# Performance work log

Measured on AMD Instinct MI355X. Metric: run time of the kernel, lower is better.

## Reference

```python
import jax, jax.numpy as jnp
import numpy as np

BOHR_RADIUS = 0.529177  # Angstrom
KE_KCAL = 332.0636      # Coulomb constant, kcal/mol * Angstrom / e^2
EPS = 1e-15
R_CUT = 5.0

ZBL = {'d': [0.8854 * BOHR_RADIUS], 'z_exp': [0.23],
       'c': [0.1818, 0.5099, 0.2802, 0.02817],
       'exponents': [3.2, 0.9423, 0.4028, 0.2016]}

def _inv_softplus(v):
    v = np.asarray(v, dtype=np.float32)
    return jnp.asarray(np.log(np.exp(v) - 1.0).reshape(-1, 1))

def setup_inputs() -> dict:
    key = jax.random.key(0)
    k1, k2, k3, k4 = jax.random.split(key, 4)
    N, E, M = 200000, 8000000, 1000
    xyz = jax.random.normal(k1, (N, 3), dtype=jnp.float32) * 3.0
    z = jax.random.randint(k2, (N,), 1, 94, dtype=jnp.int32)
    nbrs = jax.random.randint(k3, (E, 2), 0, N, dtype=jnp.int32)
    offsets = jax.random.normal(k4, (E, 3), dtype=jnp.float32) * 2.0
    num_atoms = jnp.full((M,), N // M, dtype=jnp.int32)
    return {
        'xyz': xyz, 'z': z, 'nbrs': nbrs, 'num_atoms': num_atoms, 'offsets': offsets,
        'd_inv': _inv_softplus(ZBL['d']),
        'z_exp_inv': _inv_softplus(ZBL['z_exp']),
        'c_inv': _inv_softplus(ZBL['c']),
        'exponents_inv': _inv_softplus(ZBL['exponents']),
    }

def reference(xyz, z, nbrs, num_atoms, offsets, d_inv, z_exp_inv, c_inv, exponents_inv):
    sp = jax.nn.softplus
    d, z_exp, c, exponents = sp(d_inv), sp(z_exp_inv), sp(c_inv), sp(exponents_inv)

    i, j = nbrs[:, 0], nbrs[:, 1]
    mask = j > i  # undirected-edge filter (masked instead of gathered: same math)

    z_i = z[i].astype(jnp.float32)  # [E]
    z_j = z[j].astype(jnp.float32)
    diff = xyz[i] - xyz[j] - offsets                  # [E,3]
    r_ij = jnp.sqrt((diff ** 2 + EPS).sum(-1))        # stable norm, [E]

    # ZBL phi: d,z_exp are [1,1]; broadcast over edges
    a = (d / (z_i ** z_exp + z_j ** z_exp)).reshape(-1)           # [E]
    phi = (c * jnp.exp(-exponents * r_ij / a)).sum(0) / c.sum()   # [4,E] -> [E]

    # SpookyNet cutoff, NaN-safe outside r_cut
    den = (R_CUT - r_ij) * (R_CUT + r_ij)
    safe_den = jnp.where(r_ij < R_CUT, den, 1.0)
    f_cut = jnp.where(r_ij < R_CUT, jnp.exp(-r_ij ** 2 / safe_den), 0.0)

    pairwise = KE_KCAL * z_i * z_j / r_ij * phi * f_cut
    pairwise = jnp.where(mask, pairwise, 0.0)

    N = xyz.shape[0]
    M = num_atoms.shape[0]
    mol_idx = jnp.repeat(jnp.arange(M), num_atoms, total_repeat_length=N)  # [N]
    seg = mol_idx[i]                                                       # [E]
    energy = jax.ops.segment_sum(pairwise, seg, num_segments=M).reshape(-1, 1)
    return energy
```

## Files before the change

kernel.cpp:

```cpp
#include <hip/hip_runtime.h>
#include <hip/hip_bf16.h>

#define KE_F     332.0636f
#define MAX_M    1024
#define BLK      256
#define NBLK_MAX 2048

__device__ __forceinline__ float softplusf(float x) {
    return logf(1.0f + expf(x));
}

__global__ void scan_params_kernel(const int* __restrict__ num_atoms, int M,
                                   const float* __restrict__ d_inv,
                                   const float* __restrict__ z_exp_inv,
                                   const float* __restrict__ c_inv,
                                   const float* __restrict__ exp_inv,
                                   int* __restrict__ mol_starts,
                                   float* __restrict__ params) {
    __shared__ int buf[MAX_M];
    int t = threadIdx.x;
    buf[t] = (t < M) ? num_atoms[t] : 0;
    __syncthreads();
    for (int off = 1; off < MAX_M; off <<= 1) {
        int x = (t >= off) ? buf[t - off] : 0;
        __syncthreads();
        buf[t] += x;
        __syncthreads();
    }
    if (t == 0) mol_starts[0] = 0;
    if (t < M) mol_starts[t + 1] = buf[t];
    if (t == 0) {
        float dd = softplusf(d_inv[0]);
        float c0 = softplusf(c_inv[0]), c1 = softplusf(c_inv[1]);
        float c2 = softplusf(c_inv[2]), c3 = softplusf(c_inv[3]);
        float e0 = softplusf(exp_inv[0]), e1 = softplusf(exp_inv[1]);
        float e2 = softplusf(exp_inv[2]), e3 = softplusf(exp_inv[3]);
        float ic = 1.0f / (c0 + c1 + c2 + c3);
        float id = 1.0f / dd;
        params[0] = c0 * ic; params[1] = c1 * ic; params[2] = c2 * ic; params[3] = c3 * ic;
        params[4] = e0 * id; params[5] = e1 * id; params[6] = e2 * id; params[7] = e3 * id;
        params[8] = softplusf(z_exp_inv[0]);
    }
}

__global__ void pack_kernel(const float* __restrict__ xyz,
                            const int* __restrict__ z,
                            const int* __restrict__ mol_starts, int M, int N,
                            const float* __restrict__ params,
                            float4* __restrict__ pack,
                            float2* __restrict__ aux) {
    int a = blockIdx.x * blockDim.x + threadIdx.x;
    if (a >= N) return;
    float zf = (float)z[a];
    pack[a] = make_float4(xyz[3 * a + 0], xyz[3 * a + 1], xyz[3 * a + 2], zf);
    int lo = 0, hi = M;
    while (hi - lo > 1) {
        int mid = (lo + hi) >> 1;
        if (mol_starts[mid] <= a) lo = mid; else hi = mid;
    }
    aux[a] = make_float2(__powf(zf, params[8]), __int_as_float(lo));
}

__global__ __launch_bounds__(256) void nr_main_kernel(
    const long long* __restrict__ nbrs,
    const float* __restrict__ offsets,
    const float4* __restrict__ pack,
    const float2* __restrict__ aux,
    const float* __restrict__ params,
    float* __restrict__ part, int E) {
    __shared__ float sm[MAX_M];
    for (int t = threadIdx.x; t < MAX_M; t += BLK) sm[t] = 0.0f;
    __syncthreads();

    const float4 kk = *(const float4*)(params + 0);
    const float4 gg = *(const float4*)(params + 4);

    const int stride = gridDim.x * BLK;
    for (int e = blockIdx.x * BLK + threadIdx.x; e < E; e += stride) {
        const long long nb = __builtin_nontemporal_load(nbrs + e);
        const int i = (int)nb;
        const int j = (int)(nb >> 32);
        if (j <= i) continue;

        const float ox = __builtin_nontemporal_load(offsets + 3 * e + 0);
        const float oy = __builtin_nontemporal_load(offsets + 3 * e + 1);
        const float oz = __builtin_nontemporal_load(offsets + 3 * e + 2);
        const float4 pi = pack[i];
        const float4 pj = pack[j];
        const float dx = pi.x - pj.x - ox;
        const float dy = pi.y - pj.y - oy;
        const float dz = pi.z - pj.z - oz;
        const float r2 = fmaf(dx, dx, fmaf(dy, dy, dz * dz)) + 3e-15f;
        if (r2 >= 25.0f) continue;

        const float inv_r = rsqrtf(r2);
        const float r = r2 * inv_r;
        const float2 ai = aux[i];
        const float2 aj = aux[j];
        const float rs = r * (ai.x + aj.x);
        const float phi = kk.x * __expf(-gg.x * rs) + kk.y * __expf(-gg.y * rs) +
                          kk.z * __expf(-gg.z * rs) + kk.w * __expf(-gg.w * rs);
        const float fcut = __expf(-__fdividef(r2, 25.0f - r2));
        const float val = KE_F * pi.w * pj.w * inv_r * phi * fcut;

        atomicAdd(&sm[__float_as_int(ai.y)], val);
    }
    __syncthreads();
    const float4* sm4 = (const float4*)sm;
    float4* dst = (float4*)(part + (size_t)blockIdx.x * MAX_M);
    dst[threadIdx.x] = sm4[threadIdx.x];
}

__global__ void reduce_kernel(const float* __restrict__ part, int nblk,
                              float* __restrict__ out, int M) {
    __shared__ float4 smr[BLK];
    const int q = blockIdx.x;
    float4 acc = make_float4(0.f, 0.f, 0.f, 0.f);
    for (int b = threadIdx.x; b < nblk; b += BLK) {
        const float4 v = *(const float4*)(part + (size_t)b * MAX_M + 4 * q);
        acc.x += v.x; acc.y += v.y; acc.z += v.z; acc.w += v.w;
    }
    smr[threadIdx.x] = acc;
    __syncthreads();
    for (int s = BLK / 2; s > 0; s >>= 1) {
        if (threadIdx.x < s) {
            smr[threadIdx.x].x += smr[threadIdx.x + s].x;
            smr[threadIdx.x].y += smr[threadIdx.x + s].y;
            smr[threadIdx.x].z += smr[threadIdx.x + s].z;
            smr[threadIdx.x].w += smr[threadIdx.x + s].w;
        }
        __syncthreads();
    }
    if (threadIdx.x == 0) {
        const int m = 4 * q;
        const float4 r = smr[0];
        if (m + 0 < M) out[m + 0] = r.x;
        if (m + 1 < M) out[m + 1] = r.y;
        if (m + 2 < M) out[m + 2] = r.z;
        if (m + 3 < M) out[m + 3] = r.w;
    }
}

extern "C" void kernel_launch(void* const* d_in, const int* in_sizes, int n_in,
                              void* d_out, int out_size, void* d_ws, size_t ws_size,
                              hipStream_t stream) {
    const float* xyz       = (const float*)d_in[0];
    const int*   z         = (const int*)d_in[1];
    const int*   nbrs      = (const int*)d_in[2];
    const int*   num_atoms = (const int*)d_in[3];
    const float* offsets   = (const float*)d_in[4];
    const float* d_inv     = (const float*)d_in[5];
    const float* z_exp_inv = (const float*)d_in[6];
    const float* c_inv     = (const float*)d_in[7];
    const float* exp_inv   = (const float*)d_in[8];
    float* out = (float*)d_out;

    const int N = in_sizes[0] / 3;
    const int E = in_sizes[2] / 2;
    const int M = in_sizes[3];

    char* w = (char*)d_ws;
    int*    mol_starts = (int*)w;
    float*  params     = (float*)(w + 4096);
    float4* pack       = (float4*)(w + 8192);
    float2* aux        = (float2*)(w + 8192 + 16 * (size_t)N);
    size_t  part_off   = 8192 + 24 * (size_t)N;
    float*  part       = (float*)(w + part_off);

    int nblk = NBLK_MAX;
    if (ws_size > part_off) {
        size_t maxb = (ws_size - part_off) / (sizeof(float) * MAX_M);
        if ((size_t)nblk > maxb) nblk = (int)maxb;
    } else {
        nblk = 1;
    }
    if (nblk < 1) nblk = 1;

    scan_params_kernel<<<1, MAX_M, 0, stream>>>(num_atoms, M, d_inv, z_exp_inv,
                                                c_inv, exp_inv, mol_starts, params);
    pack_kernel<<<(N + BLK - 1) / BLK, BLK, 0, stream>>>(xyz, z, mol_starts, M, N,
                                                         params, pack, aux);
    nr_main_kernel<<<nblk, BLK, 0, stream>>>((const long long*)nbrs, offsets,
                                             pack, aux, params, part, E);
    reduce_kernel<<<(M + 3) / 4, BLK, 0, stream>>>(part, nblk, out, M);
}
```

Before: 277.2 us.

## Process four edges per thread with vector loads, drop reduce kernel via atomics

The main kernel now handles four edges per thread using 128-bit nontemporal loads for neighbor indices and offsets. It issues all gathers up front and masks invalid edges instead of branching. z^z_exp moves into a 96-entry shared lookup table, and the molecule index goes into a separate int array. The separate reduction kernel is replaced by global atomicAdd of per-block shared sums into an output zeroed in the scan kernel. This removes one launch and the partial-sum traffic, at the cost of computing masked edges and contention on global atomics.

```diff
diff --git a/kernel.cpp b/kernel.cpp
--- a/kernel.cpp
+++ b/kernel.cpp
@@ -1,10 +1,13 @@
 #include <hip/hip_runtime.h>
 #include <hip/hip_bf16.h>
 
-#define KE_F     332.0636f
-#define MAX_M    1024
-#define BLK      256
-#define NBLK_MAX 2048
+#define KE_F  332.0636f
+#define MAX_M 1024
+#define BLK   256
+#define NBLK  2048
+
+typedef int   ivec4 __attribute__((ext_vector_type(4)));
+typedef float fvec4 __attribute__((ext_vector_type(4)));
 
 __device__ __forceinline__ float softplusf(float x) {
     return logf(1.0f + expf(x));
@@ -16,7 +19,8 @@
                                    const float* __restrict__ c_inv,
                                    const float* __restrict__ exp_inv,
                                    int* __restrict__ mol_starts,
-                                   float* __restrict__ params) {
+                                   float* __restrict__ params,
+                                   float* __restrict__ out) {
     __shared__ int buf[MAX_M];
     int t = threadIdx.x;
     buf[t] = (t < M) ? num_atoms[t] : 0;
@@ -39,105 +43,116 @@
         float id = 1.0f / dd;
         params[0] = c0 * ic; params[1] = c1 * ic; params[2] = c2 * ic; params[3] = c3 * ic;
         params[4] = e0 * id; params[5] = e1 * id; params[6] = e2 * id; params[7] = e3 * id;
-        params[8] = softplusf(z_exp_inv[0]);
     }
+    if (t < 96) {
+        float zexp = softplusf(z_exp_inv[0]);
+        params[16 + t] = __powf((float)t, zexp);
+    }
+    for (int k = t; k < M; k += MAX_M) out[k] = 0.0f;
 }
 
 __global__ void pack_kernel(const float* __restrict__ xyz,
                             const int* __restrict__ z,
                             const int* __restrict__ mol_starts, int M, int N,
-                            const float* __restrict__ params,
-                            float4* __restrict__ pack,
-                            float2* __restrict__ aux) {
+                            float4* __restrict__ pack, int* __restrict__ mol) {
     int a = blockIdx.x * blockDim.x + threadIdx.x;
     if (a >= N) return;
-    float zf = (float)z[a];
-    pack[a] = make_float4(xyz[3 * a + 0], xyz[3 * a + 1], xyz[3 * a + 2], zf);
+    pack[a] = make_float4(xyz[3 * a + 0], xyz[3 * a + 1], xyz[3 * a + 2],
+                          (float)z[a]);
     int lo = 0, hi = M;
     while (hi - lo > 1) {
         int mid = (lo + hi) >> 1;
         if (mol_starts[mid] <= a) lo = mid; else hi = mid;
     }
-    aux[a] = make_float2(__powf(zf, params[8]), __int_as_float(lo));
+    mol[a] = lo;
 }
 
-__global__ __launch_bounds__(256) void nr_main_kernel(
-    const long long* __restrict__ nbrs,
-    const float* __restrict__ offsets,
-    const float4* __restrict__ pack,
-    const float2* __restrict__ aux,
-    const float* __restrict__ params,
-    float* __restrict__ part, int E) {
+__global__ __launch_bounds__(BLK) void nr_main_kernel(
+    const int* __restrict__ nbrs, const float* __restrict__ offsets,
+    const float4* __restrict__ pack, const int* __restrict__ mol,
+    const float* __restrict__ params, float* __restrict__ out, int E, int M) {
     __shared__ float sm[MAX_M];
+    __shared__ float zp[96];
     for (int t = threadIdx.x; t < MAX_M; t += BLK) sm[t] = 0.0f;
+    if (threadIdx.x < 96) zp[threadIdx.x] = params[16 + threadIdx.x];
     __syncthreads();
 
     const float4 kk = *(const float4*)(params + 0);
     const float4 gg = *(const float4*)(params + 4);
 
+    const int ngroups = E >> 2;
     const int stride = gridDim.x * BLK;
-    for (int e = blockIdx.x * BLK + threadIdx.x; e < E; e += stride) {
-        const long long nb = __builtin_nontemporal_load(nbrs + e);
-        const int i = (int)nb;
-        const int j = (int)(nb >> 32);
+    const ivec4* nb4 = (const ivec4*)nbrs;
+    const fvec4* of4 = (const fvec4*)offsets;
+
+    for (int g = blockIdx.x * BLK + threadIdx.x; g < ngroups; g += stride) {
+        const ivec4 n01 = __builtin_nontemporal_load(nb4 + 2 * (size_t)g);
+        const ivec4 n23 = __builtin_nontemporal_load(nb4 + 2 * (size_t)g + 1);
+        const fvec4 oA  = __builtin_nontemporal_load(of4 + 3 * (size_t)g);
+        const fvec4 oB  = __builtin_nontemporal_load(of4 + 3 * (size_t)g + 1);
+        const fvec4 oC  = __builtin_nontemporal_load(of4 + 3 * (size_t)g + 2);
+
+        const int   iv[4] = {n01.x, n01.z, n23.x, n23.z};
+        const int   jv[4] = {n01.y, n01.w, n23.y, n23.w};
+        const float ox[4] = {oA.x, oA.w, oB.z, oC.y};
+        const float oy[4] = {oA.y, oB.x, oB.w, oC.z};
+        const float oz[4] = {oA.z, oB.y, oC.x, oC.w};
+
+        bool   m[4];
+        float4 pi[4], pj[4];
+        int    mi[4];
+#pragma unroll
+        for (int k = 0; k < 4; ++k) {
+            m[k] = jv[k] > iv[k];
+            const int ii = m[k] ? iv[k] : 0;
+            const int jj = m[k] ? jv[k] : 0;
+            pi[k] = pack[ii];
+            pj[k] = pack[jj];
+            mi[k] = mol[ii];
+        }
+#pragma unroll
+        for (int k = 0; k < 4; ++k) {
+            const float dx = pi[k].x - pj[k].x - ox[k];
+            const float dy = pi[k].y - pj[k].y - oy[k];
+            const float dz = pi[k].z - pj[k].z - oz[k];
+            const float r2 = fmaf(dx, dx, fmaf(dy, dy, dz * dz)) + 3e-15f;
+            const bool ok = m[k] && (r2 < 25.0f);
+            const float inv_r = rsqrtf(r2);
+            const float r = r2 * inv_r;
+            const float S = zp[(int)pi[k].w] + zp[(int)pj[k].w];
+            const float rs = r * S;
+            const float phi = kk.x * __expf(-gg.x * rs) + kk.y * __expf(-gg.y * rs) +
+                              kk.z * __expf(-gg.z * rs) + kk.w * __expf(-gg.w * rs);
+            const float fc = __expf(-__fdividef(r2, 25.0f - r2));
+            const float val = KE_F * pi[k].w * pj[k].w * inv_r * phi * fc;
+            if (ok) atomicAdd(&sm[mi[k]], val);
+        }
+    }
+
+    for (int e = (ngroups << 2) + blockIdx.x * BLK + threadIdx.x; e < E; e += stride) {
+        const int i = nbrs[2 * e], j = nbrs[2 * e + 1];
         if (j <= i) continue;
-
-        const float ox = __builtin_nontemporal_load(offsets + 3 * e + 0);
-        const float oy = __builtin_nontemporal_load(offsets + 3 * e + 1);
-        const float oz = __builtin_nontemporal_load(offsets + 3 * e + 2);
-        const float4 pi = pack[i];
-        const float4 pj = pack[j];
-        const float dx = pi.x - pj.x - ox;
-        const float dy = pi.y - pj.y - oy;
-        const float dz = pi.z - pj.z - oz;
+        const float oxs = offsets[3 * e], oys = offsets[3 * e + 1], ozs = offsets[3 * e + 2];
+        const float4 pis = pack[i], pjs = pack[j];
+        const float dx = pis.x - pjs.x - oxs;
+        const float dy = pis.y - pjs.y - oys;
+        const float dz = pis.z - pjs.z - ozs;
         const float r2 = fmaf(dx, dx, fmaf(dy, dy, dz * dz)) + 3e-15f;
         if (r2 >= 25.0f) continue;
-
         const float inv_r = rsqrtf(r2);
         const float r = r2 * inv_r;
-        const float2 ai = aux[i];
-        const float2 aj = aux[j];
-        const float rs = r * (ai.x + aj.x);
+        const float S = zp[(int)pis.w] + zp[(int)pjs.w];
+        const float rs = r * S;
         const float phi = kk.x * __expf(-gg.x * rs) + kk.y * __expf(-gg.y * rs) +
                           kk.z * __expf(-gg.z * rs) + kk.w * __expf(-gg.w * rs);
-        const float fcut = __expf(-__fdividef(r2, 25.0f - r2));
-        const float val = KE_F * pi.w * pj.w * inv_r * phi * fcut;
+        const float fc = __expf(-__fdividef(r2, 25.0f - r2));
+        atomicAdd(&sm[mol[i]], KE_F * pis.w * pjs.w * inv_r * phi * fc);
+    }
 
-        atomicAdd(&sm[__float_as_int(ai.y)], val);
-    }
     __syncthreads();
-    const float4* sm4 = (const float4*)sm;
-    float4* dst = (float4*)(part + (size_t)blockIdx.x * MAX_M);
-    dst[threadIdx.x] = sm4[threadIdx.x];
-}
-
-__global__ void reduce_kernel(const float* __restrict__ part, int nblk,
-                              float* __restrict__ out, int M) {
-    __shared__ float4 smr[BLK];
-    const int q = blockIdx.x;
-    float4 acc = make_float4(0.f, 0.f, 0.f, 0.f);
-    for (int b = threadIdx.x; b < nblk; b += BLK) {
-        const float4 v = *(const float4*)(part + (size_t)b * MAX_M + 4 * q);
-        acc.x += v.x; acc.y += v.y; acc.z += v.z; acc.w += v.w;
-    }
-    smr[threadIdx.x] = acc;
-    __syncthreads();
-    for (int s = BLK / 2; s > 0; s >>= 1) {
-        if (threadIdx.x < s) {
-            smr[threadIdx.x].x += smr[threadIdx.x + s].x;
-            smr[threadIdx.x].y += smr[threadIdx.x + s].y;
-            smr[threadIdx.x].z += smr[threadIdx.x + s].z;
-            smr[threadIdx.x].w += smr[threadIdx.x + s].w;
-        }
-        __syncthreads();
-    }
-    if (threadIdx.x == 0) {
-        const int m = 4 * q;
-        const float4 r = smr[0];
-        if (m + 0 < M) out[m + 0] = r.x;
-        if (m + 1 < M) out[m + 1] = r.y;
-        if (m + 2 < M) out[m + 2] = r.z;
-        if (m + 3 < M) out[m + 3] = r.w;
+    for (int t = threadIdx.x; t < M; t += BLK) {
+        const float v = sm[t];
+        if (v != 0.0f) atomicAdd(&out[t], v);
     }
 }
 
@@ -163,24 +178,13 @@
     int*    mol_starts = (int*)w;
     float*  params     = (float*)(w + 4096);
     float4* pack       = (float4*)(w + 8192);
-    float2* aux        = (float2*)(w + 8192 + 16 * (size_t)N);
-    size_t  part_off   = 8192 + 24 * (size_t)N;
-    float*  part       = (float*)(w + part_off);
-
-    int nblk = NBLK_MAX;
-    if (ws_size > part_off) {
-        size_t maxb = (ws_size - part_off) / (sizeof(float) * MAX_M);
-        if ((size_t)nblk > maxb) nblk = (int)maxb;
-    } else {
-        nblk = 1;
-    }
-    if (nblk < 1) nblk = 1;
+    int*    mol        = (int*)(w + 8192 + 16 * (size_t)N);
 
     scan_params_kernel<<<1, MAX_M, 0, stream>>>(num_atoms, M, d_inv, z_exp_inv,
-                                                c_inv, exp_inv, mol_starts, params);
+                                                c_inv, exp_inv, mol_starts,
+                                                params, out);
     pack_kernel<<<(N + BLK - 1) / BLK, BLK, 0, stream>>>(xyz, z, mol_starts, M, N,
-                                                         params, pack, aux);
-    nr_main_kernel<<<nblk, BLK, 0, stream>>>((const long long*)nbrs, offsets,
-                                             pack, aux, params, part, E);
-    reduce_kernel<<<(M + 3) / 4, BLK, 0, stream>>>(part, nblk, out, M);
+                                                         pack, mol);
+    nr_main_kernel<<<NBLK, BLK, 0, stream>>>(nbrs, offsets, pack, mol,
+                                             params, out, E, M);
 }
```

Result: faster. 260.8 us (-5.9%).
